# Performance work log

Measured on AMD Instinct MI355X. Metric: run time of the kernel, lower is better.

## Reference

```python
import jax, jax.numpy as jnp
import numpy as np

B, S, H, E, K = 4, 2048, 1024, 8, 2


def setup_inputs() -> dict:
    key = jax.random.key(0)
    k0, k1, k2 = jax.random.split(key, 3)
    x = jax.random.normal(k0, (B, S, H), dtype=jnp.float32)
    # gate: Linear(H -> E); torch stores W as [out,in], we keep [E,H]
    gate_w = jax.random.normal(k1, (E, H), dtype=jnp.float32) * 0.02
    gate_b = jnp.zeros((E,), dtype=jnp.float32)
    # experts: E x Linear(H -> H); stored as [E, H_in, H_out]
    expert_w = jax.random.normal(k2, (E, H, H), dtype=jnp.float32) * 0.02
    expert_b = jnp.zeros((E, H), dtype=jnp.float32)
    return {"x": x, "gate_w": gate_w, "gate_b": gate_b,
            "expert_w": expert_w, "expert_b": expert_b}


def reference(x, gate_w, gate_b, expert_w, expert_b):
    bsz, seq_len, h = x.shape
    xt = x.reshape(-1, h)                      # [T, H]
    T = xt.shape[0]

    # router (moe_router): softmax -> top-k -> renormalize
    logits = xt @ gate_w.T + gate_b            # [T, E]
    routing_probs = jax.nn.softmax(logits, axis=-1)
    top_k_probs, top_k_index = jax.lax.top_k(routing_probs, K)
    top_k_probs = top_k_probs / jnp.sum(top_k_probs, axis=1, keepdims=True)
    top_k_probs = top_k_probs.astype(x.dtype)

    # combine weights: scatter normalized top-k probs into [T, E]
    rows = jnp.arange(T)[:, None]
    combine = jnp.zeros((T, E), dtype=x.dtype).at[rows, top_k_index].add(top_k_probs)

    # per-expert FFN over all tokens, then weighted combine
    # (equivalent math to the gather / index_add loop: zero weights contribute zero)
    y = jnp.einsum('th,eho->teo', xt, expert_w) + expert_b[None, :, :]  # [T, E, H]
    out = jnp.einsum('te,teh->th', combine, y)                          # [T, H]

    final_output = out.reshape(bsz, seq_len, h)
    return final_output, top_k_index, routing_probs
```

## Files before the change

kernel.cpp:

```cpp
#include <hip/hip_runtime.h>
#include <hip/hip_bf16.h>
#include <stdint.h>

typedef unsigned short ushort_t;
typedef __bf16 bf16x8 __attribute__((ext_vector_type(8)));
typedef float f32x4 __attribute__((ext_vector_type(4)));

#define T_TOK 8192
#define H_DIM 1024
#define E_EXP 8
#define BM 256
#define BN 256
#define BK 64
#define NKT (H_DIM / BK)
#define NITER (NKT / 2)
#define NWG_G 512

#define CNT_STRIDE 64
#define RTOK 32
#define RBLOCKS (T_TOK / RTOK)
#define TP_BLOCKS ((H_DIM / 32) * (H_DIM / 32) * E_EXP)

static __device__ __forceinline__ ushort_t f2bf(float f) {
  union { float f; uint32_t u; } c; c.f = f;
  uint32_t u = c.u;
  uint32_t r = u + 0x7FFFu + ((u >> 16) & 1u);
  return (ushort_t)(r >> 16);
}

__global__ __launch_bounds__(256) void router_transpose(
    const float* __restrict__ x, const float* __restrict__ gw,
    const float* __restrict__ gb, const float* __restrict__ ew,
    float* __restrict__ out_idx, float* __restrict__ out_probs,
    ushort_t* __restrict__ x_bf, int* __restrict__ counts,
    int* __restrict__ tok, float* __restrict__ wts, int* __restrict__ slotmap,
    ushort_t* __restrict__ wT)
{
  __shared__ int   sm_eid[RTOK * 2];
  __shared__ float sm_wt[RTOK * 2];
  __shared__ int   lcnt[E_EXP], lbase[E_EXP], lpos[E_EXP];
  __shared__ float tile[32][33];

  const int tid = threadIdx.x;

  if (blockIdx.x >= RBLOCKS) {
    const int tb = blockIdx.x - RBLOCKS;
    const int e = tb >> 10;
    const int n0 = (tb & 31) * 32, k0 = ((tb >> 5) & 31) * 32;
    const float* we = ew + (size_t)e * H_DIM * H_DIM;
    ushort_t* wTe = wT + (size_t)e * H_DIM * H_DIM;
    const int tx = tid & 31, ty = tid >> 5;
#pragma unroll
    for (int i = 0; i < 4; i++)
      tile[ty + 8 * i][tx] = we[(size_t)(k0 + ty + 8 * i) * H_DIM + n0 + tx];
    __syncthreads();
#pragma unroll
    for (int i = 0; i < 4; i++)
      wTe[(size_t)(n0 + ty + 8 * i) * H_DIM + k0 + tx] = f2bf(tile[tx][ty + 8 * i]);
    return;
  }

  const int wave = tid >> 6, l = tid & 63;
  if (tid < E_EXP) { lcnt[tid] = 0; lpos[tid] = 0; }
  __syncthreads();

  const int t0 = blockIdx.x * RTOK;
  for (int it = 0; it < RTOK / 4; it++) {
    const int lt = wave * (RTOK / 4) + it;
    const int t = t0 + lt;
    const float* xt = x + (size_t)t * H_DIM;
    float acc[E_EXP];
#pragma unroll
    for (int e = 0; e < E_EXP; e++) acc[e] = 0.f;
#pragma unroll
    for (int i = 0; i < 4; i++) {
      const int h = (i * 64 + l) * 4;
      const float4 xv = *reinterpret_cast<const float4*>(xt + h);
      ushort4 b;
      b.x = f2bf(xv.x); b.y = f2bf(xv.y); b.z = f2bf(xv.z); b.w = f2bf(xv.w);
      *reinterpret_cast<ushort4*>(x_bf + (size_t)t * H_DIM + h) = b;
#pragma unroll
      for (int e = 0; e < E_EXP; e++) {
        const float4 g = *reinterpret_cast<const float4*>(gw + e * H_DIM + h);
        acc[e] += xv.x * g.x + xv.y * g.y + xv.z * g.z + xv.w * g.w;
      }
    }
#pragma unroll
    for (int e = 0; e < E_EXP; e++) {
      float v = acc[e];
#pragma unroll
      for (int off = 32; off; off >>= 1) v += __shfl_xor(v, off);
      acc[e] = v;
    }
    if (l == 0) {
      float lg[E_EXP], pb[E_EXP];
      float m = -1e30f;
#pragma unroll
      for (int e = 0; e < E_EXP; e++) { lg[e] = acc[e] + gb[e]; m = fmaxf(m, lg[e]); }
      float s = 0.f;
#pragma unroll
      for (int e = 0; e < E_EXP; e++) { pb[e] = expf(lg[e] - m); s += pb[e]; }
      const float inv = 1.f / s;
#pragma unroll
      for (int e = 0; e < E_EXP; e++) {
        pb[e] *= inv;
        out_probs[(size_t)t * E_EXP + e] = pb[e];
      }
      int i0 = 0; float p0 = pb[0];
#pragma unroll
      for (int e = 1; e < E_EXP; e++) if (pb[e] > p0) { p0 = pb[e]; i0 = e; }
      int i1 = -1; float p1 = -1.f;
#pragma unroll
      for (int e = 0; e < E_EXP; e++) if (e != i0 && pb[e] > p1) { p1 = pb[e]; i1 = e; }
      out_idx[(size_t)t * 2 + 0] = (float)i0;
      out_idx[(size_t)t * 2 + 1] = (float)i1;
      const float rn = 1.f / (p0 + p1);
      sm_eid[lt * 2 + 0] = i0; sm_wt[lt * 2 + 0] = p0 * rn;
      sm_eid[lt * 2 + 1] = i1; sm_wt[lt * 2 + 1] = p1 * rn;
    }
  }
  __syncthreads();

  if (tid < RTOK * 2) atomicAdd(&lcnt[sm_eid[tid]], 1);
  __syncthreads();
  if (tid < E_EXP) lbase[tid] = atomicAdd(&counts[tid * CNT_STRIDE], lcnt[tid]);
  __syncthreads();
  if (tid < RTOK * 2) {
    const int e = sm_eid[tid];
    const int p = lbase[e] + atomicAdd(&lpos[e], 1);
    tok[e * T_TOK + p] = t0 + (tid >> 1);
    wts[e * T_TOK + p] = sm_wt[tid];
    slotmap[(t0 + (tid >> 1)) * 2 + (tid & 1)] = e * T_TOK + p;
  }
}

#define GLDS16(gp, lp)                                                         \
  __builtin_amdgcn_global_load_lds(                                            \
      (const __attribute__((address_space(1))) void*)(gp),                     \
      (__attribute__((address_space(3))) void*)(lp), 16, 0, 0)

#define WAITV6() asm volatile("s_waitcnt vmcnt(6)" ::: "memory")
#define WAITV0() asm volatile("s_waitcnt vmcnt(0)" ::: "memory")
#define LGKM0()                                                                \
  do {                                                                         \
    asm volatile("s_waitcnt lgkmcnt(0)" ::: "memory");                         \
    __builtin_amdgcn_sched_barrier(0);                                         \
  } while (0)
#define BAR()                                                                  \
  do {                                                                         \
    __builtin_amdgcn_sched_barrier(0);                                         \
    __builtin_amdgcn_s_barrier();                                              \
    __builtin_amdgcn_sched_barrier(0);                                         \
  } while (0)

__global__ __launch_bounds__(512, 2) void moe_gemm(
    const ushort_t* __restrict__ x_bf, const ushort_t* __restrict__ wT,
    const float* __restrict__ bias, int* __restrict__ counts,
    const int* __restrict__ tok, const float* __restrict__ wts,
    ushort_t* __restrict__ y)
{
  __shared__ __align__(16) ushort_t AsR[2 * 2 * BM * 32];
  __shared__ __align__(16) ushort_t BsR[2 * 2 * BM * 32];
  __shared__ int stok[BM];
  __shared__ float swt[BM];
  __shared__ int s_spill;
#define AS_(buf, kh, idx) AsR[((buf) * 2 + (kh)) * 8192 + (idx)]
#define BS_(buf, kh, idx) BsR[((buf) * 2 + (kh)) * 8192 + (idx)]

  const int tid = threadIdx.x;
  const int bid = blockIdx.x;

  int ne[E_EXP], fl[E_EXP];
#pragma unroll
  for (int i = 0; i < E_EXP; i++) {
    ne[i] = counts[i * CNT_STRIDE];
    fl[i] = ne[i] >> 8;
  }

  const int l = tid & 63;
  const int wid = tid >> 6;
  const int fr = l & 15;
  const int g = l >> 4;

  if (bid < 256) {
    int e = bid & 7;
    int q = bid >> 3;
    const int home = fl[e] * 4;
    if (q >= (home < 32 ? home : 32)) {
      int sc[E_EXP], spill_total = 0;
#pragma unroll
      for (int i = 0; i < E_EXP; i++) {
        sc[i] = fl[i] * 4 > 32 ? fl[i] * 4 - 32 : 0;
        spill_total += sc[i];
      }
      if (spill_total == 0) return;
      if (tid == 0) s_spill = atomicAdd(&counts[520], 1);
      __syncthreads();
      int k = s_spill;
      if (k >= spill_total) return;
      int done = 0;
#pragma unroll
      for (int i = 0; i < E_EXP; i++) {
        if (!done) { if (k < sc[i]) { e = i; done = 1; } else k -= sc[i]; }
      }
      q = 32 + k;
    }
    const int mt = q >> 2;
    const int nt = q & 3;

    if (tid < BM) {
      stok[tid] = tok[e * T_TOK + mt * BM + tid];
      swt[tid] = wts[e * T_TOK + mt * BM + tid];
    }
    __syncthreads();

    const int r0 = tid >> 2;
    const int cp = (tid & 3) ^ ((tid >> 3) & 3);
    const ushort_t* wTe = wT + (size_t)e * H_DIM * H_DIM;
    const ushort_t* aP0 = x_bf + (size_t)stok[r0] * H_DIM + cp * 8;
    const ushort_t* aP1 = x_bf + (size_t)stok[r0 + 128] * H_DIM + cp * 8;
    const ushort_t* bP0 = wTe + (size_t)(nt * BN + r0) * H_DIM + cp * 8;
    const ushort_t* bP1 = wTe + (size_t)(nt * BN + r0 + 128) * H_DIM + cp * 8;
    const int d0 = tid * 8;
    const int d1 = (tid + 512) * 8;

#define STAGE_A(t, kh, buf)                                                    \
  do {                                                                         \
    GLDS16(aP0 + (t) * BK + (kh) * 32, &AS_((buf), (kh), d0));                 \
    GLDS16(aP1 + (t) * BK + (kh) * 32, &AS_((buf), (kh), d1));                 \
  } while (0)
#define STAGE_B(t, kh, buf)                                                    \
  do {                                                                         \
    GLDS16(bP0 + (t) * BK + (kh) * 32, &BS_((buf), (kh), d0));                 \
    GLDS16(bP1 + (t) * BK + (kh) * 32, &BS_((buf), (kh), d1));                 \
  } while (0)

    const int wm = wid >> 2, wn = wid & 3;
    const int sl = g ^ ((l >> 1) & 3);
    const int arow0 = wm * 128 + fr;
    const int brow0 = wn * 64 + fr;

    bf16x8 af[8], bv[2];
    f32x4 acc[8][4] = {};

#define READ_A(buf, kk)                                                        \
  do {                                                                         \
    _Pragma("unroll") for (int mi = 0; mi < 8; mi++)                           \
        af[mi] = *reinterpret_cast<const bf16x8*>(                             \
            &AS_((buf), (kk), (arow0 + mi * 16) * 32 + sl * 8));               \
  } while (0)
#define READ_B(buf, kk, nh)                                                    \
  do {                                                                         \
    _Pragma("unroll") for (int j = 0; j < 2; j++)                              \
        bv[j] = *reinterpret_cast<const bf16x8*>(                              \
            &BS_((buf), (kk), (brow0 + ((nh) * 2 + j) * 16) * 32 + sl * 8));   \
  } while (0)
#define MFMA16(nh)                                                             \
  do {                                                                         \
    __builtin_amdgcn_s_setprio(1);                                             \
    _Pragma("unroll") for (int mi = 0; mi < 8; mi++)                           \
        _Pragma("unroll") for (int j = 0; j < 2; j++)                          \
            acc[mi][(nh) * 2 + j] = __builtin_amdgcn_mfma_f32_16x16x32_bf16(   \
                af[mi], bv[j], acc[mi][(nh) * 2 + j], 0, 0, 0);                \
    __builtin_amdgcn_s_setprio(0);                                             \
  } while (0)

#define ITER_BODY(TT, MORE)                                                    \
  do {                                                                         \
                                                                       \
    READ_A(0, 0); READ_B(0, 0, 0);                                             \
    STAGE_B((TT) + 1, 1, 1);                                                   \
    BAR(); LGKM0(); MFMA16(0); BAR();                                          \
                                                                       \
    READ_B(0, 0, 1);                                                           \
    if (MORE) STAGE_A((TT) + 2, 0, 0);                                         \
    BAR(); LGKM0(); MFMA16(1); BAR();                                          \
                                                                       \
    READ_A(0, 1); READ_B(0, 1, 0);                                             \
    if (MORE) STAGE_B((TT) + 2, 0, 0);                                         \
    BAR(); LGKM0(); MFMA16(0); BAR();                                          \
                                               \
    READ_B(0, 1, 1);                                                           \
    if (MORE) { STAGE_A((TT) + 2, 1, 0); WAITV6(); } else { WAITV0(); }        \
    BAR(); LGKM0(); MFMA16(1); BAR();                                          \
                                                                       \
    READ_A(1, 0); READ_B(1, 0, 0);                                             \
    if (MORE) STAGE_B((TT) + 2, 1, 0);                                         \
    BAR(); LGKM0(); MFMA16(0); BAR();                                          \
                                                                       \
    READ_B(1, 0, 1);                                                           \
    if (MORE) STAGE_A((TT) + 3, 0, 1);                                         \
    BAR(); LGKM0(); MFMA16(1); BAR();                                          \
                                                                       \
    READ_A(1, 1); READ_B(1, 1, 0);                                             \
    if (MORE) STAGE_B((TT) + 3, 0, 1);                                         \
    BAR(); LGKM0(); MFMA16(0); BAR();                                          \
                                               \
    READ_B(1, 1, 1);                                                           \
    if (MORE) { STAGE_A((TT) + 3, 1, 1); WAITV6(); }                           \
    BAR(); LGKM0(); MFMA16(1); BAR();                                          \
  } while (0)

    STAGE_A(0, 0, 0); STAGE_B(0, 0, 0); STAGE_A(0, 1, 0); STAGE_B(0, 1, 0);
    STAGE_A(1, 0, 1); STAGE_B(1, 0, 1); STAGE_A(1, 1, 1);
    WAITV6();
    BAR();

#pragma unroll 1
    for (int it = 0; it < NITER - 1; ++it) {
      const int t = 2 * it;
      ITER_BODY(t, 1);
    }
    {
      const int t = 2 * (NITER - 1);
      ITER_BODY(t, 0);
    }

    ushort_t* ye = y + ((size_t)e * T_TOK + (size_t)mt * BM) * H_DIM;
    float bias4[4];
#pragma unroll
    for (int nj = 0; nj < 4; nj++)
      bias4[nj] = bias[e * H_DIM + nt * BN + wn * 64 + nj * 16 + fr];
#pragma unroll
    for (int mi = 0; mi < 8; mi++) {
      const int rr0 = wm * 128 + mi * 16 + g * 4;
#pragma unroll
      for (int r = 0; r < 4; r++) {
        const int row = rr0 + r;
        const float wgt = swt[row];
#pragma unroll
        for (int nj = 0; nj < 4; nj++) {
          const int n = nt * BN + wn * 64 + nj * 16 + fr;
          ye[(size_t)row * H_DIM + n] = f2bf(wgt * (acc[mi][nj][r] + bias4[nj]));
        }
      }
    }
  } else {
    const int e = bid & 7;
    const int tq = (bid - 256) >> 3;
    const int rem = ne[e] - (fl[e] << 8);
    const int tcnt = (rem + 63) >> 6;
    if (tq >= tcnt * 8) return;
    const int mtt = tq >> 3;
    const int ntt = tq & 7;
    const int row0 = (fl[e] << 8) + mtt * 64;
    int valid = ne[e] - row0; if (valid > 64) valid = 64;

    if (tid < 64) {
      int slot = row0 + tid;
      if (slot >= ne[e]) slot = ne[e] - 1;
      stok[tid] = tok[e * T_TOK + slot];
      swt[tid] = wts[e * T_TOK + slot];
    }
    __syncthreads();

    const ushort_t* wTe = wT + (size_t)e * H_DIM * H_DIM;
    const int trow = tid >> 3;
    const int tlc = (tid & 7) ^ (trow & 7);
    const ushort_t* taS = x_bf + (size_t)stok[trow] * H_DIM + tlc * 8;
    const ushort_t* tbS0 = wTe + (size_t)(ntt * 128 + trow) * H_DIM + tlc * 8;
    const ushort_t* tbS1 = tbS0 + (size_t)64 * H_DIM;

#define TSTAGE(t, buf)                                                         \
  do {                                                                         \
    GLDS16(taS + (t) * BK, &AsR[(buf) * 4096 + tid * 8]);                      \
    GLDS16(tbS0 + (t) * BK, &BsR[(buf) * 8192 + tid * 8]);                     \
    GLDS16(tbS1 + (t) * BK, &BsR[(buf) * 8192 + (tid + 512) * 8]);             \
  } while (0)

    const int tph0 = (g ^ (fr & 7)) * 8;
    const int tph1 = ((4 ^ g) ^ (fr & 7)) * 8;

    f32x4 tacc[4] = {};

    TSTAGE(0, 0);
    WAITV0();
    BAR();

#pragma unroll
    for (int t = 0; t < NKT; ++t) {
      if (t + 1 < NKT) TSTAGE(t + 1, (t + 1) & 1);
      const ushort_t* Ab = &AsR[(t & 1) * 4096];
      const ushort_t* Bb = &BsR[(t & 1) * 8192];
#pragma unroll
      for (int kk = 0; kk < 2; kk++) {
        const int ph = kk ? tph1 : tph0;
        const bf16x8 tbv = *reinterpret_cast<const bf16x8*>(
            &Bb[(wid * 16 + fr) * 64 + ph]);
#pragma unroll
        for (int mi = 0; mi < 4; mi++) {
          const bf16x8 tav = *reinterpret_cast<const bf16x8*>(
              &Ab[(mi * 16 + fr) * 64 + ph]);
          tacc[mi] = __builtin_amdgcn_mfma_f32_16x16x32_bf16(
              tav, tbv, tacc[mi], 0, 0, 0);
        }
      }
      WAITV0();
      BAR();
    }

    ushort_t* ye = y + ((size_t)e * T_TOK + row0) * H_DIM;
    const int ncol = ntt * 128 + wid * 16 + fr;
    const float bs = bias[e * H_DIM + ncol];
#pragma unroll
    for (int mi = 0; mi < 4; mi++) {
      const int rb = mi * 16 + g * 4;
#pragma unroll
      for (int r = 0; r < 4; r++) {
        const int row = rb + r;
        if (row < valid) {
          ye[(size_t)row * H_DIM + ncol] = f2bf(swt[row] * (tacc[mi][r] + bs));
        }
      }
    }
  }
}

__global__ __launch_bounds__(256) void combine_kernel(
    const ushort_t* __restrict__ y, const int* __restrict__ slotmap,
    float* __restrict__ out)
{
  const int t = blockIdx.x;
  const int s0 = slotmap[t * 2 + 0];
  const int s1 = slotmap[t * 2 + 1];
  const ushort_t* r0 = y + (size_t)s0 * H_DIM;
  const ushort_t* r1 = y + (size_t)s1 * H_DIM;
  float* o = out + (size_t)t * H_DIM;
  const int h = threadIdx.x * 4;
  const ushort4 u0 = *reinterpret_cast<const ushort4*>(r0 + h);
  const ushort4 u1 = *reinterpret_cast<const ushort4*>(r1 + h);
  float4 v;
  union { uint32_t u; float f; } c;
  c.u = (uint32_t)u0.x << 16; v.x = c.f; c.u = (uint32_t)u1.x << 16; v.x += c.f;
  c.u = (uint32_t)u0.y << 16; v.y = c.f; c.u = (uint32_t)u1.y << 16; v.y += c.f;
  c.u = (uint32_t)u0.z << 16; v.z = c.f; c.u = (uint32_t)u1.z << 16; v.z += c.f;
  c.u = (uint32_t)u0.w << 16; v.w = c.f; c.u = (uint32_t)u1.w << 16; v.w += c.f;
  *reinterpret_cast<float4*>(o + h) = v;
}

extern "C" void kernel_launch(void* const* d_in, const int* in_sizes, int n_in,
                              void* d_out, int out_size, void* d_ws, size_t ws_size,
                              hipStream_t stream)
{
  const float* x  = (const float*)d_in[0];
  const float* gw = (const float*)d_in[1];
  const float* gb = (const float*)d_in[2];
  const float* ew = (const float*)d_in[3];
  const float* eb = (const float*)d_in[4];

  float* out = (float*)d_out;
  float* out_final = out;
  float* out_idx   = out + (size_t)T_TOK * H_DIM;
  float* out_probs = out_idx + (size_t)T_TOK * 2;

  char* ws = (char*)d_ws;
  size_t off = 0;
  int*      counts  = (int*)(ws + off); off += 4096;
  int*      tok     = (int*)(ws + off); off += (size_t)E_EXP * T_TOK * 4;
  float*    wts     = (float*)(ws + off); off += (size_t)E_EXP * T_TOK * 4;
  int*      slotmap = (int*)(ws + off); off += (size_t)T_TOK * 2 * 4;
  ushort_t* x_bf    = (ushort_t*)(ws + off); off += (size_t)T_TOK * H_DIM * 2;
  ushort_t* wT      = (ushort_t*)(ws + off); off += (size_t)E_EXP * H_DIM * H_DIM * 2;
  ushort_t* y       = (ushort_t*)(ws + off); off += (size_t)E_EXP * T_TOK * H_DIM * 2;

  hipMemsetAsync(counts, 0, 4096, stream);

  router_transpose<<<RBLOCKS + TP_BLOCKS, 256, 0, stream>>>(
      x, gw, gb, ew, out_idx, out_probs, x_bf, counts, tok, wts, slotmap, wT);
  moe_gemm<<<NWG_G, 512, 0, stream>>>(x_bf, wT, eb, counts, tok, wts, y);
  combine_kernel<<<T_TOK, 256, 0, stream>>>(y, slotmap, out_final);
}
```

Measured before the change: 95.11 us.

## Pre-gather token rows per expert in router and scatter GEMM output by slot

```diff
diff --git a/kernel.cpp b/kernel.cpp
--- a/kernel.cpp
+++ b/kernel.cpp
@@ -32,12 +32,13 @@
     const float* __restrict__ x, const float* __restrict__ gw,
     const float* __restrict__ gb, const float* __restrict__ ew,
     float* __restrict__ out_idx, float* __restrict__ out_probs,
-    ushort_t* __restrict__ x_bf, int* __restrict__ counts,
-    int* __restrict__ tok, float* __restrict__ wts, int* __restrict__ slotmap,
-    ushort_t* __restrict__ wT)
+    int* __restrict__ counts, int* __restrict__ tok, float* __restrict__ wts,
+    ushort_t* __restrict__ xg, ushort_t* __restrict__ wT)
 {
+  __shared__ ushort_t xrow[RTOK][H_DIM];
   __shared__ int   sm_eid[RTOK * 2];
   __shared__ float sm_wt[RTOK * 2];
+  __shared__ int   sm_dst[RTOK * 2];
   __shared__ int   lcnt[E_EXP], lbase[E_EXP], lpos[E_EXP];
   __shared__ float tile[32][33];
 
@@ -78,7 +79,7 @@
       const float4 xv = *reinterpret_cast<const float4*>(xt + h);
       ushort4 b;
       b.x = f2bf(xv.x); b.y = f2bf(xv.y); b.z = f2bf(xv.z); b.w = f2bf(xv.w);
-      *reinterpret_cast<ushort4*>(x_bf + (size_t)t * H_DIM + h) = b;
+      *reinterpret_cast<ushort4*>(&xrow[lt][h]) = b;
 #pragma unroll
       for (int e = 0; e < E_EXP; e++) {
         const float4 g = *reinterpret_cast<const float4*>(gw + e * H_DIM + h);
@@ -128,9 +129,22 @@
   if (tid < RTOK * 2) {
     const int e = sm_eid[tid];
     const int p = lbase[e] + atomicAdd(&lpos[e], 1);
-    tok[e * T_TOK + p] = t0 + (tid >> 1);
-    wts[e * T_TOK + p] = sm_wt[tid];
-    slotmap[(t0 + (tid >> 1)) * 2 + (tid & 1)] = e * T_TOK + p;
+    const int dst = e * T_TOK + p;
+    tok[dst] = (t0 + (tid >> 1)) * 2 + (tid & 1);
+    wts[dst] = sm_wt[tid];
+    sm_dst[tid] = dst;
+  }
+  __syncthreads();
+
+  for (int ent0 = 0; ent0 < RTOK * 2; ent0 += 4) {
+    const int ent = ent0 + wave;
+    const int dst = sm_dst[ent];
+    const ushort_t* src = &xrow[ent >> 1][0];
+    ushort_t* d = xg + (size_t)dst * H_DIM;
+    const int o = l * 16;
+    *reinterpret_cast<int4*>(d + o) = *reinterpret_cast<const int4*>(src + o);
+    *reinterpret_cast<int4*>(d + o + 8) =
+        *reinterpret_cast<const int4*>(src + o + 8);
   }
 }
 
@@ -154,7 +168,7 @@
   } while (0)
 
 __global__ __launch_bounds__(512, 2) void moe_gemm(
-    const ushort_t* __restrict__ x_bf, const ushort_t* __restrict__ wT,
+    const ushort_t* __restrict__ xg, const ushort_t* __restrict__ wT,
     const float* __restrict__ bias, int* __restrict__ counts,
     const int* __restrict__ tok, const float* __restrict__ wts,
     ushort_t* __restrict__ y)
@@ -217,8 +231,9 @@
     const int r0 = tid >> 2;
     const int cp = (tid & 3) ^ ((tid >> 3) & 3);
     const ushort_t* wTe = wT + (size_t)e * H_DIM * H_DIM;
-    const ushort_t* aP0 = x_bf + (size_t)stok[r0] * H_DIM + cp * 8;
-    const ushort_t* aP1 = x_bf + (size_t)stok[r0 + 128] * H_DIM + cp * 8;
+    const ushort_t* aBase = xg + (size_t)(e * T_TOK + mt * BM) * H_DIM;
+    const ushort_t* aP0 = aBase + (size_t)r0 * H_DIM + cp * 8;
+    const ushort_t* aP1 = aBase + (size_t)(r0 + 128) * H_DIM + cp * 8;
     const ushort_t* bP0 = wTe + (size_t)(nt * BN + r0) * H_DIM + cp * 8;
     const ushort_t* bP1 = wTe + (size_t)(nt * BN + r0 + 128) * H_DIM + cp * 8;
     const int d0 = tid * 8;
@@ -316,7 +331,6 @@
       ITER_BODY(t, 0);
     }
 
-    ushort_t* ye = y + ((size_t)e * T_TOK + (size_t)mt * BM) * H_DIM;
     float bias4[4];
 #pragma unroll
     for (int nj = 0; nj < 4; nj++)
@@ -328,10 +342,11 @@
       for (int r = 0; r < 4; r++) {
         const int row = rr0 + r;
         const float wgt = swt[row];
+        ushort_t* yr = y + (size_t)stok[row] * H_DIM;
 #pragma unroll
         for (int nj = 0; nj < 4; nj++) {
           const int n = nt * BN + wn * 64 + nj * 16 + fr;
-          ye[(size_t)row * H_DIM + n] = f2bf(wgt * (acc[mi][nj][r] + bias4[nj]));
+          yr[n] = f2bf(wgt * (acc[mi][nj][r] + bias4[nj]));
         }
       }
     }
@@ -357,7 +372,9 @@
     const ushort_t* wTe = wT + (size_t)e * H_DIM * H_DIM;
     const int trow = tid >> 3;
     const int tlc = (tid & 7) ^ (trow & 7);
-    const ushort_t* taS = x_bf + (size_t)stok[trow] * H_DIM + tlc * 8;
+    int tsl = row0 + trow;
+    if (tsl >= ne[e]) tsl = ne[e] - 1;
+    const ushort_t* taS = xg + (size_t)(e * T_TOK + tsl) * H_DIM + tlc * 8;
     const ushort_t* tbS0 = wTe + (size_t)(ntt * 128 + trow) * H_DIM + tlc * 8;
     const ushort_t* tbS1 = tbS0 + (size_t)64 * H_DIM;
 
@@ -399,7 +416,6 @@
       BAR();
     }
 
-    ushort_t* ye = y + ((size_t)e * T_TOK + row0) * H_DIM;
     const int ncol = ntt * 128 + wid * 16 + fr;
     const float bs = bias[e * H_DIM + ncol];
 #pragma unroll
@@ -409,7 +425,8 @@
       for (int r = 0; r < 4; r++) {
         const int row = rb + r;
         if (row < valid) {
-          ye[(size_t)row * H_DIM + ncol] = f2bf(swt[row] * (tacc[mi][r] + bs));
+          ushort_t* yr = y + (size_t)stok[row] * H_DIM;
+          yr[ncol] = f2bf(swt[row] * (tacc[mi][r] + bs));
         }
       }
     }
@@ -417,14 +434,11 @@
 }
 
 __global__ __launch_bounds__(256) void combine_kernel(
-    const ushort_t* __restrict__ y, const int* __restrict__ slotmap,
-    float* __restrict__ out)
+    const ushort_t* __restrict__ y, float* __restrict__ out)
 {
   const int t = blockIdx.x;
-  const int s0 = slotmap[t * 2 + 0];
-  const int s1 = slotmap[t * 2 + 1];
-  const ushort_t* r0 = y + (size_t)s0 * H_DIM;
-  const ushort_t* r1 = y + (size_t)s1 * H_DIM;
+  const ushort_t* r0 = y + (size_t)(t * 2) * H_DIM;
+  const ushort_t* r1 = r0 + H_DIM;
   float* o = out + (size_t)t * H_DIM;
   const int h = threadIdx.x * 4;
   const ushort4 u0 = *reinterpret_cast<const ushort4*>(r0 + h);
@@ -458,15 +472,14 @@
   int*      counts  = (int*)(ws + off); off += 4096;
   int*      tok     = (int*)(ws + off); off += (size_t)E_EXP * T_TOK * 4;
   float*    wts     = (float*)(ws + off); off += (size_t)E_EXP * T_TOK * 4;
-  int*      slotmap = (int*)(ws + off); off += (size_t)T_TOK * 2 * 4;
-  ushort_t* x_bf    = (ushort_t*)(ws + off); off += (size_t)T_TOK * H_DIM * 2;
   ushort_t* wT      = (ushort_t*)(ws + off); off += (size_t)E_EXP * H_DIM * H_DIM * 2;
-  ushort_t* y       = (ushort_t*)(ws + off); off += (size_t)E_EXP * T_TOK * H_DIM * 2;
+  ushort_t* y       = (ushort_t*)(ws + off); off += (size_t)T_TOK * 2 * H_DIM * 2;
+  ushort_t* xg      = (ushort_t*)(ws + off); off += (size_t)E_EXP * T_TOK * H_DIM * 2;
 
   hipMemsetAsync(counts, 0, 4096, stream);
 
   router_transpose<<<RBLOCKS + TP_BLOCKS, 256, 0, stream>>>(
-      x, gw, gb, ew, out_idx, out_probs, x_bf, counts, tok, wts, slotmap, wT);
-  moe_gemm<<<NWG_G, 512, 0, stream>>>(x_bf, wT, eb, counts, tok, wts, y);
-  combine_kernel<<<T_TOK, 256, 0, stream>>>(y, slotmap, out_final);
+      x, gw, gb, ew, out_idx, out_probs, counts, tok, wts, xg, wT);
+  moe_gemm<<<NWG_G, 512, 0, stream>>>(xg, wT, eb, counts, tok, wts, y);
+  combine_kernel<<<T_TOK, 256, 0, stream>>>(y, out_final);
 }
```

New measurement: 97.56 us. 2.6% more time.
